# Performance work log

Measured on AMD Instinct MI355X. Metric: run time of the kernel, lower is better.

## Reference

```python
import jax, jax.numpy as jnp
import numpy as np

N = 100000  # nodes


def _gcn_prep(edge_index):
    # PyG GCNConv(normalize=True): add self loops, symmetric deg^{-1/2} norm.
    row = jnp.concatenate([edge_index[0], jnp.arange(N, dtype=edge_index.dtype)])
    col = jnp.concatenate([edge_index[1], jnp.arange(N, dtype=edge_index.dtype)])
    deg = jax.ops.segment_sum(jnp.ones(row.shape[0], dtype=jnp.float32), col, num_segments=N)
    deg_isqrt = jnp.where(deg > 0, jax.lax.rsqrt(jnp.maximum(deg, 1.0)), 0.0)
    norm = deg_isqrt[row] * deg_isqrt[col]  # [E+N]
    return row, col, norm


def _gcn_conv(x, W, b, row, col, norm):
    h = x @ W                                  # [N, out]
    msg = h[row] * norm[:, None]               # [E+N, out] gather + scale
    out = jax.ops.segment_sum(msg, col, num_segments=N)  # scatter-add
    return out + b


def setup_inputs() -> dict:
    key = jax.random.key(0)
    ks = jax.random.split(key, 7)
    E = 3200000
    x = jax.random.normal(ks[0], (N, 100), dtype=jnp.float32)
    edge_index = jax.random.randint(ks[1], (2, E), 0, N, dtype=jnp.int32)
    def glorot(k, fi, fo):
        s = (6.0 / (fi + fo)) ** 0.5
        return jax.random.uniform(k, (fi, fo), jnp.float32, -s, s)
    return {
        "x": x, "edge_index": edge_index,
        "W1": glorot(ks[2], 100, 64), "b1": jnp.zeros((64,), jnp.float32),
        "W2": glorot(ks[3], 64, 64),  "b2": jnp.zeros((64,), jnp.float32),
        "W3": glorot(ks[4], 64, 64),  "b3": jnp.zeros((64,), jnp.float32),
        "Wo": glorot(ks[5], 64, 18),  "bo": jnp.zeros((18,), jnp.float32),
    }


def reference(x, edge_index, W1, b1, W2, b2, W3, b3, Wo, bo):
    row, col, norm = _gcn_prep(edge_index)
    # eval mode: F.dropout(training=False) is identity
    h = jax.nn.relu(_gcn_conv(x, W1, b1, row, col, norm))
    h = jax.nn.relu(_gcn_conv(h, W2, b2, row, col, norm))
    h = jax.nn.relu(_gcn_conv(h, W3, b3, row, col, norm))
    return _gcn_conv(h, Wo, bo, row, col, norm)
```

## Files before the change

### kernel.cpp

```cpp
#include <hip/hip_runtime.h>
#include <hip/hip_fp16.h>

#define NODES 100000
#define NBKT 782
#define HCHUNK 8192
#define FCHUNK 4096

typedef unsigned short u16;
typedef unsigned int u32;

__device__ __forceinline__ float bflo(u32 v) { return __uint_as_float(v << 16); }
__device__ __forceinline__ float bfhi(u32 v) { return __uint_as_float(v & 0xFFFF0000u); }
__device__ __forceinline__ u16 f2bf(float f) {
  u32 x = __float_as_uint(f);
  return (u16)((x + 0x7FFFu + ((x >> 16) & 1u)) >> 16);
}


__global__ __launch_bounds__(256) void zero_k(int* __restrict__ p, int n) {
  int i = blockIdx.x * 256 + threadIdx.x;
  if (i < n) p[i] = 0;
}


__global__ __launch_bounds__(256) void bucket_hist_k(const int* __restrict__ col,
                                                     int* __restrict__ bcnt, int E) {
  __shared__ int h[NBKT];
  int t = threadIdx.x;
  for (int i = t; i < NBKT; i += 256) h[i] = 0;
  __syncthreads();
  int base = blockIdx.x * HCHUNK;
#pragma unroll 4
  for (int j = 0; j < HCHUNK / 256; ++j) {
    int i = base + j * 256 + t;
    if (i < E) atomicAdd(&h[col[i] >> 7], 1);
  }
  __syncthreads();
  for (int i = t; i < NBKT; i += 256) {
    int c = h[i];
    if (c) atomicAdd(&bcnt[i], c);
  }
}

__global__ __launch_bounds__(256) void bscan_k(const int* __restrict__ bcnt,
                                               int* __restrict__ boffs,
                                               int* __restrict__ bcurs, int nb, int E) {
  __shared__ int lds[256];
  int t = threadIdx.x;
  int base = t * 4;
  int v[4];
#pragma unroll
  for (int j = 0; j < 4; ++j) v[j] = (base + j < nb) ? bcnt[base + j] : 0;
  int s = v[0] + v[1] + v[2] + v[3];
  lds[t] = s;
  __syncthreads();
  for (int off = 1; off < 256; off <<= 1) {
    int y = (t >= off) ? lds[t - off] : 0;
    __syncthreads();
    lds[t] += y;
    __syncthreads();
  }
  int excl = lds[t] - s;
#pragma unroll
  for (int j = 0; j < 4; ++j) {
    int i = base + j;
    if (i < nb) { boffs[i] = excl; bcurs[i] = excl; }
    excl += v[j];
  }
  if (t == 255) boffs[nb] = E;
}

__global__ __launch_bounds__(256) void bucket_fill_k(const int* __restrict__ row,
                                                     const int* __restrict__ col,
                                                     int* __restrict__ bcurs,
                                                     u32* __restrict__ recs, int E) {
  __shared__ int lcnt[NBKT];
  __shared__ int lbase[NBKT];
  int t = threadIdx.x;
  int base = blockIdx.x * FCHUNK;
  for (int i = t; i < NBKT; i += 256) lcnt[i] = 0;
  __syncthreads();
  u32 rec[FCHUNK / 256];
  u32 meta[FCHUNK / 256];
#pragma unroll
  for (int j = 0; j < FCHUNK / 256; ++j) {
    int i = base + j * 256 + t;
    if (i < E) {
      int r = row[i], c = col[i];
      int b = c >> 7;
      rec[j] = (u32)r | ((u32)(c & 127) << 17);
      int lr = atomicAdd(&lcnt[b], 1);
      meta[j] = (u32)lr | ((u32)b << 16);
    } else {
      meta[j] = 0xFFFFFFFFu;
    }
  }
  __syncthreads();
  for (int i = t; i < NBKT; i += 256) {
    int c = lcnt[i];
    lbase[i] = c ? atomicAdd(&bcurs[i], c) : 0;
  }
  __syncthreads();
#pragma unroll
  for (int j = 0; j < FCHUNK / 256; ++j) {
    if (meta[j] != 0xFFFFFFFFu) {
      int b = meta[j] >> 16;
      int lr = meta[j] & 0xFFFF;
      recs[lbase[b] + lr] = rec[j];
    }
  }
}

__global__ __launch_bounds__(256) void csr_k(const u32* __restrict__ recs,
                                             const int* __restrict__ boffs,
                                             int* __restrict__ offs, int* __restrict__ adj,
                                             float* __restrict__ dis, int N, int E) {
  __shared__ int cnt[128];
  __shared__ int sa[128], sb[128];
  __shared__ int cur[128];
  int b = blockIdx.x, t = threadIdx.x;
  if (t < 128) cnt[t] = 0;
  __syncthreads();
  int s = boffs[b], e = boffs[b + 1];
  for (int i = s + t; i < e; i += 256) atomicAdd(&cnt[recs[i] >> 17], 1);
  __syncthreads();
  if (t < 128) sa[t] = cnt[t];
  __syncthreads();
#pragma unroll
  for (int off = 1; off < 128; off <<= 1) {
    if (t < 128) sb[t] = sa[t] + ((t >= off) ? sa[t - off] : 0);
    __syncthreads();
    if (t < 128) sa[t] = sb[t];
    __syncthreads();
  }
  if (t < 128) {
    int c = b * 128 + t;
    if (c < N) {
      int excl = sa[t] - cnt[t];
      offs[c] = s + excl;
      cur[t] = s + excl;
      dis[c] = rsqrtf((float)(cnt[t] + 1));
    }
  }
  if (b == 0 && t == 0) offs[N] = E;
  __syncthreads();
  for (int i = s + t; i < e; i += 256) {
    u32 r = recs[i];
    int p = atomicAdd(&cur[r >> 17], 1);
    adj[p] = (int)(r & 0x1FFFF);
  }
}

template <int K, int XS, int NOUT, int CH, int OUTFMT>
__global__ __launch_bounds__(256) void gemm_scale_k(const float* __restrict__ X,
                                                    const float* __restrict__ W,
                                                    const float* __restrict__ dis,
                                                    void* __restrict__ G, int n) {
  __shared__ float Xs[64 * XS];
  __shared__ float Ws[K * NOUT + 8];
  int t = threadIdx.x;
  int b0 = blockIdx.x * 64;
  for (int i = t; i < K * NOUT; i += 256) Ws[i] = W[i];
  int lim = n * K;
  for (int i = t; i < 64 * K; i += 256) {
    int r = i / K, c = i - r * K;
    int gi = b0 * K + i;
    Xs[r * XS + c] = (gi < lim) ? X[gi] : 0.f;
  }
  __syncthreads();
  int nl = t >> 2, ch = t & 3;
  float acc[CH];
#pragma unroll
  for (int j = 0; j < CH; ++j) acc[j] = 0.f;
  const float* xr = &Xs[nl * XS];
  const float* wc = &Ws[ch * CH];
  for (int k = 0; k < K; ++k) {
    float a = xr[k];
#pragma unroll
    for (int j = 0; j < CH; ++j) acc[j] = fmaf(a, wc[k * NOUT + j], acc[j]);
  }
  __syncthreads();
  int node = b0 + nl;
  float s = (node < n) ? dis[node] : 0.f;
  constexpr int ST = NOUT + 1;
#pragma unroll
  for (int j = 0; j < CH; ++j) {
    int jj = ch * CH + j;
    if (jj < NOUT) Xs[nl * ST + jj] = acc[j] * s;
  }
  __syncthreads();
  int gbase = b0 * NOUT;
  int glim = n * NOUT;
  for (int i = t; i < 64 * NOUT; i += 256) {
    int r = i / NOUT, c = i - r * NOUT;
    if (gbase + i < glim) {
      float v = Xs[r * ST + c];
      if (OUTFMT == 1)      ((u16*)G)[gbase + i] = f2bf(v);
      else if (OUTFMT == 2) ((u16*)G)[gbase + i] = __half_as_ushort(__float2half(v));
      else                  ((float*)G)[gbase + i] = v;
    }
  }
}

__global__ __launch_bounds__(256) void agg_bf16_k(const u16* __restrict__ g,
                                                  const int* __restrict__ offs,
                                                  const int* __restrict__ adj,
                                                  const float* __restrict__ dis,
                                                  const float* __restrict__ bias,
                                                  float* __restrict__ out, int n) {
  int node = blockIdx.x * 4 + (threadIdx.x >> 6);
  int lane = threadIdx.x & 63;
  int half = lane >> 5, fl = lane & 31;
  if (node >= n) return;
  const u32* g32 = (const u32*)g;
  float acc0 = 0.f, acc1 = 0.f;
  int s = offs[node], e = offs[node + 1];
  int i = s;
  for (; i + 16 <= e; i += 16) {
    int r0 = adj[i + half];
    int r1 = adj[i + 2 + half];
    int r2 = adj[i + 4 + half];
    int r3 = adj[i + 6 + half];
    int r4 = adj[i + 8 + half];
    int r5 = adj[i + 10 + half];
    int r6 = adj[i + 12 + half];
    int r7 = adj[i + 14 + half];
    u32 v0 = g32[(r0 << 5) + fl];
    u32 v1 = g32[(r1 << 5) + fl];
    u32 v2 = g32[(r2 << 5) + fl];
    u32 v3 = g32[(r3 << 5) + fl];
    u32 v4 = g32[(r4 << 5) + fl];
    u32 v5 = g32[(r5 << 5) + fl];
    u32 v6 = g32[(r6 << 5) + fl];
    u32 v7 = g32[(r7 << 5) + fl];
    acc0 += ((bflo(v0) + bflo(v1)) + (bflo(v2) + bflo(v3))) +
            ((bflo(v4) + bflo(v5)) + (bflo(v6) + bflo(v7)));
    acc1 += ((bfhi(v0) + bfhi(v1)) + (bfhi(v2) + bfhi(v3))) +
            ((bfhi(v4) + bfhi(v5)) + (bfhi(v6) + bfhi(v7)));
  }
  for (; i + 8 <= e; i += 8) {
    int r0 = adj[i + half];
    int r1 = adj[i + 2 + half];
    int r2 = adj[i + 4 + half];
    int r3 = adj[i + 6 + half];
    u32 v0 = g32[(r0 << 5) + fl];
    u32 v1 = g32[(r1 << 5) + fl];
    u32 v2 = g32[(r2 << 5) + fl];
    u32 v3 = g32[(r3 << 5) + fl];
    acc0 += (bflo(v0) + bflo(v1)) + (bflo(v2) + bflo(v3));
    acc1 += (bfhi(v0) + bfhi(v1)) + (bfhi(v2) + bfhi(v3));
  }
  for (; i + 2 <= e; i += 2) {
    int r = adj[i + half];
    u32 v = g32[(r << 5) + fl];
    acc0 += bflo(v);
    acc1 += bfhi(v);
  }
  if (i < e) {
    int r = adj[i];
    u32 v = g32[(r << 5) + fl];
    if (half == 0) { acc0 += bflo(v); acc1 += bfhi(v); }
  }
  acc0 += __shfl_xor(acc0, 32, 64);
  acc1 += __shfl_xor(acc1, 32, 64);
  u32 vs = g32[(node << 5) + fl];
  acc0 += bflo(vs);
  acc1 += bfhi(vs);
  float d = dis[node];
  float o0 = fmaxf(fmaf(d, acc0, bias[2 * fl]), 0.f);
  float o1 = fmaxf(fmaf(d, acc1, bias[2 * fl + 1]), 0.f);
  if (half == 0) {
    float2 st = {o0, o1};
    *(float2*)(out + node * 64 + 2 * fl) = st;
  }
}

__global__ __launch_bounds__(256) void agg_f16o_k(const u16* __restrict__ g,
                                                  const int* __restrict__ offs,
                                                  const int* __restrict__ adj,
                                                  const float* __restrict__ dis,
                                                  const float* __restrict__ bias,
                                                  float* __restrict__ out, int n) {
  int node = blockIdx.x * 4 + (threadIdx.x >> 6);
  int lane = threadIdx.x & 63;
  int half = lane >> 5, fl = lane & 31;
  if (node >= n) return;
  const __half* gh = (const __half*)g;
  bool act = fl < 18;
  float acc = 0.f;
  int s = offs[node], e = offs[node + 1];
  int i = s;
  if (act) {
    for (; i + 16 <= e; i += 16) {
      int r0 = adj[i + half];
      int r1 = adj[i + 2 + half];
      int r2 = adj[i + 4 + half];
      int r3 = adj[i + 6 + half];
      int r4 = adj[i + 8 + half];
      int r5 = adj[i + 10 + half];
      int r6 = adj[i + 12 + half];
      int r7 = adj[i + 14 + half];
      float a0 = __half2float(gh[r0 * 18 + fl]);
      float a1 = __half2float(gh[r1 * 18 + fl]);
      float a2 = __half2float(gh[r2 * 18 + fl]);
      float a3 = __half2float(gh[r3 * 18 + fl]);
      float a4 = __half2float(gh[r4 * 18 + fl]);
      float a5 = __half2float(gh[r5 * 18 + fl]);
      float a6 = __half2float(gh[r6 * 18 + fl]);
      float a7 = __half2float(gh[r7 * 18 + fl]);
      acc += ((a0 + a1) + (a2 + a3)) + ((a4 + a5) + (a6 + a7));
    }
    for (; i + 8 <= e; i += 8) {
      int r0 = adj[i + half];
      int r1 = adj[i + 2 + half];
      int r2 = adj[i + 4 + half];
      int r3 = adj[i + 6 + half];
      float a0 = __half2float(gh[r0 * 18 + fl]);
      float a1 = __half2float(gh[r1 * 18 + fl]);
      float a2 = __half2float(gh[r2 * 18 + fl]);
      float a3 = __half2float(gh[r3 * 18 + fl]);
      acc += (a0 + a1) + (a2 + a3);
    }
    for (; i + 2 <= e; i += 2) acc += __half2float(gh[adj[i + half] * 18 + fl]);
    if (i < e && half == 0) acc += __half2float(gh[adj[i] * 18 + fl]);
  }
  acc += __shfl_xor(acc, 32, 64);
  if (act) {
    acc += __half2float(gh[node * 18 + fl]);
    float v = fmaf(dis[node], acc, bias[fl]);
    if (half == 0) out[node * 18 + fl] = v;
  }
}


extern "C" void kernel_launch(void* const* d_in, const int* in_sizes, int n_in,
                              void* d_out, int out_size, void* d_ws, size_t ws_size,
                              hipStream_t stream) {
  const float* x  = (const float*)d_in[0];
  const int*   ei = (const int*)d_in[1];
  const float* W1 = (const float*)d_in[2];
  const float* b1 = (const float*)d_in[3];
  const float* W2 = (const float*)d_in[4];
  const float* b2 = (const float*)d_in[5];
  const float* W3 = (const float*)d_in[6];
  const float* b3 = (const float*)d_in[7];
  const float* Wo = (const float*)d_in[8];
  const float* bo = (const float*)d_in[9];
  float* out = (float*)d_out;

  const int N = NODES;
  const int E = in_sizes[1] / 2;
  const int* rowp = ei;
  const int* colp = ei + E;

  char* p = (char*)d_ws;
  auto alloc = [&](size_t bytes) {
    void* r = (void*)p;
    p += (bytes + 255) & ~(size_t)255;
    return r;
  };
  int*   bcnt  = (int*)alloc((size_t)NBKT * 4);
  int*   bcurs = (int*)alloc((size_t)NBKT * 4);
  int*   boffs = (int*)alloc((size_t)(NBKT + 1) * 4);
  float* dis   = (float*)alloc((size_t)N * 4);
  int*   offs  = (int*)alloc((size_t)(N + 1) * 4);
  int*   adj   = (int*)alloc((size_t)E * 4);
  u32*   recs  = (u32*)alloc((size_t)N * 64 * 2);
  u16*   gb    = (u16*)recs;
  float* h     = (float*)alloc((size_t)N * 64 * 4);
  u16*   g4    = (u16*)alloc((size_t)N * 18 * 2);

  zero_k<<<(NBKT + 255) / 256, 256, 0, stream>>>(bcnt, NBKT);
  bucket_hist_k<<<(E + HCHUNK - 1) / HCHUNK, 256, 0, stream>>>(colp, bcnt, E);
  bscan_k<<<1, 256, 0, stream>>>(bcnt, boffs, bcurs, NBKT, E);
  bucket_fill_k<<<(E + FCHUNK - 1) / FCHUNK, 256, 0, stream>>>(rowp, colp, bcurs, recs, E);
  csr_k<<<NBKT, 256, 0, stream>>>(recs, boffs, offs, adj, dis, N, E);

  int gG = (N + 63) / 64;
  int gA = (N + 3) / 4;

  gemm_scale_k<100, 100, 64, 16, 1><<<gG, 256, 0, stream>>>(x, W1, dis, gb, N);
  agg_bf16_k<<<gA, 256, 0, stream>>>(gb, offs, adj, dis, b1, h, N);

  gemm_scale_k<64, 65, 64, 16, 1><<<gG, 256, 0, stream>>>(h, W2, dis, gb, N);
  agg_bf16_k<<<gA, 256, 0, stream>>>(gb, offs, adj, dis, b2, h, N);

  gemm_scale_k<64, 65, 64, 16, 1><<<gG, 256, 0, stream>>>(h, W3, dis, gb, N);
  agg_bf16_k<<<gA, 256, 0, stream>>>(gb, offs, adj, dis, b3, h, N);

  gemm_scale_k<64, 65, 18, 5, 2><<<gG, 256, 0, stream>>>(h, Wo, dis, g4, N);
  agg_f16o_k<<<gA, 256, 0, stream>>>(g4, offs, adj, dis, bo, out, N);
}
```

Before: 494.5 us.

## Rewrite dense GEMM as one-node-per-thread wave kernel with scalar weight loads

Replaces the 256-thread GEMM, which staged W in LDS and split each node's outputs across four threads, with a 64-thread kernel where each thread computes all outputs for one node. W is read straight from global memory with uniform addresses, so the compiler can use scalar loads. X is loaded with float4, and the output is packed into bf16/fp16 pairs in LDS before a coalesced u32 store. This removes the LDS traffic for W and most of the index arithmetic, but it needs 64 accumulator registers per thread and runs only one wave per block.

New measurement: 539.0 us. +9.0%, slower.

```diff
diff --git a/kernel.cpp b/kernel.cpp
--- a/kernel.cpp
+++ b/kernel.cpp
@@ -151,54 +151,67 @@
   }
 }
 
-template <int K, int XS, int NOUT, int CH, int OUTFMT>
-__global__ __launch_bounds__(256) void gemm_scale_k(const float* __restrict__ X,
-                                                    const float* __restrict__ W,
-                                                    const float* __restrict__ dis,
-                                                    void* __restrict__ G, int n) {
-  __shared__ float Xs[64 * XS];
-  __shared__ float Ws[K * NOUT + 8];
+template <int K, int KP, int NOUT, int OUTFMT>
+__global__ __launch_bounds__(64) void gemm_sw_k(const float* __restrict__ X,
+                                                const float* __restrict__ W,
+                                                const float* __restrict__ dis,
+                                                u16* __restrict__ G, int n) {
+  __shared__ float Xs[64 * KP];
   int t = threadIdx.x;
   int b0 = blockIdx.x * 64;
-  for (int i = t; i < K * NOUT; i += 256) Ws[i] = W[i];
-  int lim = n * K;
-  for (int i = t; i < 64 * K; i += 256) {
-    int r = i / K, c = i - r * K;
-    int gi = b0 * K + i;
-    Xs[r * XS + c] = (gi < lim) ? X[gi] : 0.f;
-  }
-  __syncthreads();
-  int nl = t >> 2, ch = t & 3;
-  float acc[CH];
-#pragma unroll
-  for (int j = 0; j < CH; ++j) acc[j] = 0.f;
-  const float* xr = &Xs[nl * XS];
-  const float* wc = &Ws[ch * CH];
+  constexpr int NF4 = K / 4;
+  const float4* X4 = (const float4*)X;
+  int base4 = b0 * NF4;
+  int lim4 = (n * K) >> 2;
+  for (int i = t; i < 64 * NF4; i += 64) {
+    float4 v = {0.f, 0.f, 0.f, 0.f};
+    if (base4 + i < lim4) v = X4[base4 + i];
+    int r = i / NF4, c4 = i - r * NF4;
+    ((float4*)Xs)[r * (KP / 4) + c4] = v;
+  }
+  __syncthreads();
+
+  float acc[NOUT];
+#pragma unroll
+  for (int j = 0; j < NOUT; ++j) acc[j] = 0.f;
+  const float* xr = &Xs[t * KP];
+#pragma unroll 2
   for (int k = 0; k < K; ++k) {
     float a = xr[k];
 #pragma unroll
-    for (int j = 0; j < CH; ++j) acc[j] = fmaf(a, wc[k * NOUT + j], acc[j]);
-  }
-  __syncthreads();
-  int node = b0 + nl;
-  float s = (node < n) ? dis[node] : 0.f;
-  constexpr int ST = NOUT + 1;
-#pragma unroll
-  for (int j = 0; j < CH; ++j) {
-    int jj = ch * CH + j;
-    if (jj < NOUT) Xs[nl * ST + jj] = acc[j] * s;
-  }
-  __syncthreads();
-  int gbase = b0 * NOUT;
-  int glim = n * NOUT;
-  for (int i = t; i < 64 * NOUT; i += 256) {
-    int r = i / NOUT, c = i - r * NOUT;
-    if (gbase + i < glim) {
-      float v = Xs[r * ST + c];
-      if (OUTFMT == 1)      ((u16*)G)[gbase + i] = f2bf(v);
-      else if (OUTFMT == 2) ((u16*)G)[gbase + i] = __half_as_ushort(__float2half(v));
-      else                  ((float*)G)[gbase + i] = v;
-    }
+    for (int j = 0; j < NOUT; ++j) acc[j] = fmaf(a, W[k * NOUT + j], acc[j]);
+  }
+
+  __syncthreads();
+  int node = b0 + t;
+  float sc = (node < n) ? dis[node] : 0.f;
+  if (NOUT == 64) {
+    u32* os = (u32*)Xs;
+#pragma unroll
+    for (int j = 0; j < 32; ++j) {
+      float v0 = acc[2 * j] * sc, v1 = acc[2 * j + 1] * sc;
+      u16 lo, hi;
+      if (OUTFMT == 1) { lo = f2bf(v0); hi = f2bf(v1); }
+      else { lo = __half_as_ushort(__float2half(v0)); hi = __half_as_ushort(__float2half(v1)); }
+      os[t * 33 + j] = (u32)lo | ((u32)hi << 16);
+    }
+    __syncthreads();
+    u32* G32 = (u32*)G;
+    for (int idx = t; idx < 64 * 32; idx += 64) {
+      int r = idx >> 5;
+      if (b0 + r < n) G32[(size_t)b0 * 32 + idx] = os[r * 33 + (idx & 31)];
+    }
+  } else {
+    u16* s16 = (u16*)Xs;
+#pragma unroll
+    for (int j = 0; j < NOUT; ++j) {
+      float v = acc[j] * sc;
+      s16[t * NOUT + j] = (OUTFMT == 1) ? f2bf(v) : __half_as_ushort(__float2half(v));
+    }
+    __syncthreads();
+    int nn = n - b0; if (nn > 64) nn = 64;
+    int lim2 = nn * NOUT;
+    for (int idx = t; idx < lim2; idx += 64) G[(size_t)b0 * NOUT + idx] = s16[idx];
   }
 }
 
@@ -379,15 +392,15 @@
   int gG = (N + 63) / 64;
   int gA = (N + 3) / 4;
 
-  gemm_scale_k<100, 100, 64, 16, 1><<<gG, 256, 0, stream>>>(x, W1, dis, gb, N);
+  gemm_sw_k<100, 100, 64, 1><<<gG, 64, 0, stream>>>(x, W1, dis, gb, N);
   agg_bf16_k<<<gA, 256, 0, stream>>>(gb, offs, adj, dis, b1, h, N);
 
-  gemm_scale_k<64, 65, 64, 16, 1><<<gG, 256, 0, stream>>>(h, W2, dis, gb, N);
+  gemm_sw_k<64, 68, 64, 1><<<gG, 64, 0, stream>>>(h, W2, dis, gb, N);
   agg_bf16_k<<<gA, 256, 0, stream>>>(gb, offs, adj, dis, b2, h, N);
 
-  gemm_scale_k<64, 65, 64, 16, 1><<<gG, 256, 0, stream>>>(h, W3, dis, gb, N);
+  gemm_sw_k<64, 68, 64, 1><<<gG, 64, 0, stream>>>(h, W3, dis, gb, N);
   agg_bf16_k<<<gA, 256, 0, stream>>>(gb, offs, adj, dis, b3, h, N);
 
-  gemm_scale_k<64, 65, 18, 5, 2><<<gG, 256, 0, stream>>>(h, Wo, dis, g4, N);
+  gemm_sw_k<64, 68, 18, 2><<<gG, 64, 0, stream>>>(h, Wo, dis, g4, N);
   agg_f16o_k<<<gA, 256, 0, stream>>>(g4, offs, adj, dis, bo, out, N);
 }
```
